# Kernel optimization log

Hardware: AMD Instinct MI355X
Metric: run time of the kernel (lower is better)

Reference implementation:

```python
import jax, jax.numpy as jnp
import numpy as np

HQ, HK, HD, DM = 16, 8, 128, 2048
GQA = HQ // HK
SCALE = HD ** -0.5


def _rotate_half(x):
    half = x.shape[-1] // 2
    return jnp.concatenate([-x[..., half:], x[..., :half]], axis=-1)


def _rope_tables(T, d, base=10000.0):
    inv_freq = 1.0 / (base ** (np.arange(0, d // 2, dtype=np.float32) * 2.0 / d))
    ang = np.arange(T, dtype=np.float32)[:, None] * inv_freq[None, :]  # [T, d/2]
    ang = np.concatenate([ang, ang], axis=-1)                          # [T, d]
    cos = jnp.asarray(np.cos(ang))[None, None]                         # [1,1,T,d]
    sin = jnp.asarray(np.sin(ang))[None, None]
    return cos, sin


def setup_inputs() -> dict:
    key = jax.random.key(0)
    ks = jax.random.split(key, 8)
    B, T, L = 1, 2048, 4
    x = jax.random.normal(ks[0], (B, T, DM), dtype=jnp.float32)
    depth_k = jax.random.normal(ks[1], (L, B, HK, T, HD), dtype=jnp.float32)
    depth_v = jax.random.normal(ks[2], (L, B, HK, T, HD), dtype=jnp.float32)
    cos, sin = _rope_tables(T, HD)
    Wq = jax.random.normal(ks[3], (DM, HQ * HD), dtype=jnp.float32) * 0.02
    Wk = jax.random.normal(ks[4], (DM, HK * HD), dtype=jnp.float32) * 0.02
    Wv = jax.random.normal(ks[5], (DM, HK * HD), dtype=jnp.float32) * 0.02
    Wo = jax.random.normal(ks[6], (HQ * HD, DM), dtype=jnp.float32) * 0.02
    return {"x": x, "depth_k": depth_k, "depth_v": depth_v, "cos": cos, "sin": sin,
            "Wq": Wq, "Wk": Wk, "Wv": Wv, "Wo": Wo}


def reference(x, depth_k, depth_v, cos, sin, Wq, Wk, Wv, Wo):
    B, T, D = x.shape
    # Projections -> [B, H, T, d]
    Q = (x @ Wq).reshape(B, T, HQ, HD).transpose(0, 2, 1, 3)
    K = (x @ Wk).reshape(B, T, HK, HD).transpose(0, 2, 1, 3)
    V = (x @ Wv).reshape(B, T, HK, HD).transpose(0, 2, 1, 3)
    # RoPE
    Q = Q * cos + _rotate_half(Q) * sin
    K = K * cos + _rotate_half(K) * sin
    # GQA expand (repeat_interleave along head axis)
    K_e = jnp.repeat(K, GQA, axis=1)
    V_e = jnp.repeat(V, GQA, axis=1)
    # Sequence logits with causal mask: [B, Hq, T, T]
    seq_logits = jnp.einsum('bhid,bhjd->bhij', Q, K_e) * SCALE
    causal = jnp.triu(jnp.ones((T, T), dtype=bool), k=1)
    seq_logits = jnp.where(causal[None, None], -jnp.inf, seq_logits)
    # Depth KVs: [L,B,Hk,T,d] -> [B,Hk,T,L,d] -> expand heads
    Kd = jnp.repeat(jnp.transpose(depth_k, (1, 2, 3, 0, 4)), GQA, axis=1)
    Vd = jnp.repeat(jnp.transpose(depth_v, (1, 2, 3, 0, 4)), GQA, axis=1)
    depth_logits = jnp.einsum('bhid,bhild->bhil', Q, Kd) * SCALE  # [B,Hq,T,L]
    # Joint softmax over sequence + depth positions
    combined = jnp.concatenate([seq_logits, depth_logits], axis=-1)
    weights = jax.nn.softmax(combined, axis=-1)
    seq_contrib = jnp.einsum('bhij,bhjd->bhid', weights[..., :T], V_e)
    depth_contrib = jnp.einsum('bhil,bhild->bhid', weights[..., T:], Vd)
    out = (seq_contrib + depth_contrib).transpose(0, 2, 1, 3).reshape(B, T, HQ * HD)
    return out @ Wo
```

## Files before the change

### kernel.cpp

```cpp
#include <hip/hip_runtime.h>
#include <hip/hip_bf16.h>
#include <math.h>

#define T_SEQ 2048
#define DMODEL 2048
#define NHQ 16
#define NHK 8
#define HDIM 128
#define NL 4
#define ATT_SCALE 0.08838834764831845f

typedef __attribute__((ext_vector_type(8))) short bf16x8;
typedef __attribute__((ext_vector_type(4))) float f32x4;

__device__ __forceinline__ float bf2f(short u) {
    union { float f; unsigned int i; } x;
    x.i = ((unsigned int)(unsigned short)u) << 16;
    return x.f;
}
__device__ __forceinline__ unsigned short f2bf(float f) {
    __hip_bfloat16 h = __float2bfloat16(f);
    return *reinterpret_cast<unsigned short*>(&h);
}
__device__ __forceinline__ void gload16(const void* g, void* l) {
    __builtin_amdgcn_global_load_lds(
        (const __attribute__((address_space(1))) void*)g,
        (__attribute__((address_space(3))) void*)l, 16, 0, 0);
}

__global__ __launch_bounds__(256) void cast_f32_bf16(
    const float* __restrict__ s, unsigned short* __restrict__ d)
{
    int i = blockIdx.x * 256 + threadIdx.x;
    float4 a = ((const float4*)s)[2 * i];
    float4 b = ((const float4*)s)[2 * i + 1];
    bf16x8 v;
    v[0] = (short)f2bf(a.x); v[1] = (short)f2bf(a.y);
    v[2] = (short)f2bf(a.z); v[3] = (short)f2bf(a.w);
    v[4] = (short)f2bf(b.x); v[5] = (short)f2bf(b.y);
    v[6] = (short)f2bf(b.z); v[7] = (short)f2bf(b.w);
    ((bf16x8*)d)[i] = v;
}

__global__ __launch_bounds__(256) void tcast(
    const float* __restrict__ src, unsigned short* __restrict__ dst,
    int Nsrc, int Ksrc, int dstOff)
{
    __shared__ float ls[64][65];
    const int k0 = blockIdx.x * 64, n0 = blockIdx.y * 64;
    const int tid = threadIdx.x;
    #pragma unroll
    for (int it = 0; it < 4; ++it) {
        int fi = tid + it * 256;
        int r = fi >> 4;
        int c = (fi & 15) * 4;
        float4 v = *(const float4*)&src[(size_t)(k0 + r) * Nsrc + n0 + c];
        ls[r][c] = v.x; ls[r][c + 1] = v.y; ls[r][c + 2] = v.z; ls[r][c + 3] = v.w;
    }
    __syncthreads();
    int n = tid & 63, kc = tid >> 6;
    bf16x8 v0, v1;
    #pragma unroll
    for (int j = 0; j < 8; ++j) v0[j] = (short)f2bf(ls[kc * 16 + j][n]);
    #pragma unroll
    for (int j = 0; j < 8; ++j) v1[j] = (short)f2bf(ls[kc * 16 + 8 + j][n]);
    size_t drow = (size_t)(dstOff + n0 + n) * Ksrc + k0 + kc * 16;
    *(bf16x8*)&dst[drow] = v0;
    *(bf16x8*)&dst[drow + 8] = v1;
}

__global__ __launch_bounds__(256, 4) void gemm_bt(
    const unsigned short* __restrict__ A, const unsigned short* __restrict__ Bt,
    float* __restrict__ Cf, unsigned short* __restrict__ Cq,
    unsigned short* __restrict__ Ck, unsigned short* __restrict__ Cv,
    int mode, int K)
{
    __shared__ char As[16384];
    __shared__ char Bs[8192];
    const int tid = threadIdx.x;
    const int wv = tid >> 6, lane = tid & 63;
    const int l15 = lane & 15, lg = lane >> 4;
    const int wm = wv >> 1, wn = wv & 1;
    const int bm = blockIdx.y * 128, bn = blockIdx.x * 64;

    f32x4 acc[4][2];
    #pragma unroll
    for (int i = 0; i < 4; ++i)
        #pragma unroll
        for (int j = 0; j < 2; ++j)
            acc[i][j] = (f32x4){0.f, 0.f, 0.f, 0.f};

    for (int k0 = 0; k0 < K; k0 += 64) {
        #pragma unroll
        for (int it = 0; it < 4; ++it) {
            int o = it * 4096 + tid * 16;
            int row = o >> 7;
            int sch = ((o >> 4) & 7) ^ (row & 7);
            gload16((const char*)A + ((((size_t)(bm + row) * K) + k0 + sch * 8) << 1),
                    As + it * 4096 + wv * 1024);
        }
        #pragma unroll
        for (int it = 0; it < 2; ++it) {
            int o = it * 4096 + tid * 16;
            int row = o >> 7;
            int sch = ((o >> 4) & 7) ^ (row & 7);
            gload16((const char*)Bt + ((((size_t)(bn + row) * K) + k0 + sch * 8) << 1),
                    Bs + it * 4096 + wv * 1024);
        }
        __syncthreads();
        #pragma unroll
        for (int kk = 0; kk < 2; ++kk) {
            bf16x8 av[4], bv[2];
            #pragma unroll
            for (int f = 0; f < 4; ++f) {
                int ra = wm * 64 + f * 16 + l15;
                av[f] = *(const bf16x8*)(As + ra * 128 + ((((kk << 2) | lg) ^ (ra & 7)) << 4));
            }
            #pragma unroll
            for (int f = 0; f < 2; ++f) {
                int rb = wn * 32 + f * 16 + l15;
                bv[f] = *(const bf16x8*)(Bs + rb * 128 + ((((kk << 2) | lg) ^ (rb & 7)) << 4));
            }
            #pragma unroll
            for (int mf = 0; mf < 4; ++mf)
                #pragma unroll
                for (int nf = 0; nf < 2; ++nf)
                    acc[mf][nf] = __builtin_amdgcn_mfma_f32_16x16x32_bf16(
                        av[mf], bv[nf], acc[mf][nf], 0, 0, 0);
        }
        __syncthreads();
    }

    #pragma unroll
    for (int mf = 0; mf < 4; ++mf) {
        int m0 = bm + wm * 64 + mf * 16 + lg * 4;
        #pragma unroll
        for (int nf = 0; nf < 2; ++nf) {
            int n0 = bn + wn * 32 + nf * 16 + l15;
            if (mode == 0) {
                #pragma unroll
                for (int r = 0; r < 4; ++r)
                    Cf[(size_t)(m0 + r) * 2048 + n0] = acc[mf][nf][r];
            } else if (n0 < 2048) {
                #pragma unroll
                for (int r = 0; r < 4; ++r)
                    Cq[(size_t)(m0 + r) * 2048 + n0] = f2bf(acc[mf][nf][r]);
            } else if (n0 < 3072) {
                #pragma unroll
                for (int r = 0; r < 4; ++r)
                    Ck[(size_t)(m0 + r) * 1024 + (n0 - 2048)] = f2bf(acc[mf][nf][r]);
            } else {
                ushort4 u;
                u.x = f2bf(acc[mf][nf][0]); u.y = f2bf(acc[mf][nf][1]);
                u.z = f2bf(acc[mf][nf][2]); u.w = f2bf(acc[mf][nf][3]);
                *(ushort4*)&Cv[(size_t)(n0 - 3072) * 2048 + m0] = u;
            }
        }
    }
}

__global__ __launch_bounds__(256) void rope_bf16(
    unsigned short* __restrict__ P, const float* __restrict__ cosT,
    const float* __restrict__ sinT, int H)
{
    int idx = blockIdx.x * 256 + threadIdx.x;
    int d = idx & 63;
    int h = (idx >> 6) % H;
    int t = idx / (64 * H);
    float c = cosT[t * HDIM + d];
    float s = sinT[t * HDIM + d];
    unsigned short* row = P + (size_t)t * (H * HDIM) + h * HDIM;
    float x0 = bf2f((short)row[d]), x1 = bf2f((short)row[d + 64]);
    row[d]      = f2bf(x0 * c - x1 * s);
    row[d + 64] = f2bf(x1 * c + x0 * s);
}

__global__ __launch_bounds__(256, 4) void attn_seg(
    const unsigned short* __restrict__ Qb, const unsigned short* __restrict__ Kb,
    const unsigned short* __restrict__ Vt,
    const float* __restrict__ Dk, const float* __restrict__ Dv,
    unsigned short* __restrict__ Opart, float2* __restrict__ mlpart)
{
    __shared__ char Ks[2][8192];
    __shared__ char Vs[2][8192];
    __shared__ char Ps[4096];

    const int bid = blockIdx.x;
    const int hk = bid & 7;
    const int idx = bid >> 3;
    const int hq = hk * 2 + (idx & 1);
    const int si = 79 - (idx >> 1);
    int qt, seg;
    if (si < 8)       { qt = si;            seg = 0; }
    else if (si < 24) { int v = si - 8;  qt = 8  + (v >> 1); seg = v & 1; }
    else if (si < 48) { int v = si - 24; int q3 = v / 3; qt = 16 + q3; seg = v - q3 * 3; }
    else              { int v = si - 48; qt = 24 + (v >> 2); seg = v & 3; }
    const int q0 = qt * 64;
    const int keys = q0 + 64;
    const int jbeg = seg * 512;
    const int jend = min(jbeg + 512, keys);

    const int tid = threadIdx.x;
    const int wv = tid >> 6, lane = tid & 63;
    const int l15 = lane & 15, lg = lane >> 4;
    const size_t DSTRIDE = (size_t)NHK * T_SEQ * HDIM;

    const int tq = q0 + wv * 16 + l15;
    const int qmax = q0 + wv * 16 + 15;

    bf16x8 qf[4];
    {
        const unsigned short* qrow = Qb + (size_t)tq * DMODEL + hq * HDIM;
        #pragma unroll
        for (int c = 0; c < 4; ++c)
            qf[c] = *(const bf16x8*)(qrow + c * 32 + lg * 8);
    }

    f32x4 oacc[8];
    #pragma unroll
    for (int dt = 0; dt < 8; ++dt) oacc[dt] = (f32x4){0.f, 0.f, 0.f, 0.f};
    float m = -1e30f, l = 0.f;

    #define STAGE(J0, BUF)                                                        \
        {                                                                         \
            _Pragma("unroll")                                                     \
            for (int it = 0; it < 2; ++it) {                                      \
                int o = it * 4096 + tid * 16;                                     \
                int rk = o >> 8, ck = (o >> 4) & 15;                              \
                gload16((const char*)Kb +                                         \
                        (((size_t)((J0) + rk) * 1024 + hk * 128 +                 \
                          ((ck ^ (rk & 7)) << 3)) << 1),                          \
                        Ks[BUF] + it * 4096 + wv * 1024);                         \
                int rv = o >> 6, cv = (o >> 4) & 3;                               \
                gload16((const char*)Vt +                                         \
                        (((size_t)(hk * 128 + rv) * 2048 + (J0) +                 \
                          ((cv ^ ((rv >> 1) & 3)) << 3)) << 1),                   \
                        Vs[BUF] + it * 4096 + wv * 1024);                         \
            }                                                                     \
        }

    STAGE(jbeg, 0);
    __syncthreads();
    int buf = 0;

    for (int j0 = jbeg; j0 < jend; j0 += 32) {
        if (j0 + 32 < jend) STAGE(j0 + 32, buf ^ 1);

        if (j0 <= qmax) {
            const char* ksb = Ks[buf];
            const char* vsb = Vs[buf];
            float p[2][4];
            #pragma unroll
            for (int s = 0; s < 2; ++s) {
                if (j0 + s * 16 <= qmax) {
                    f32x4 sa = (f32x4){0.f, 0.f, 0.f, 0.f};
                    int row = s * 16 + l15;
                    #pragma unroll
                    for (int c = 0; c < 4; ++c) {
                        int ch = (c * 4 + lg) ^ (row & 7);
                        bf16x8 kf = *(const bf16x8*)(ksb + row * 256 + ch * 16);
                        sa = __builtin_amdgcn_mfma_f32_16x16x32_bf16(kf, qf[c], sa, 0, 0, 0);
                    }
                    #pragma unroll
                    for (int r = 0; r < 4; ++r) {
                        int key = j0 + s * 16 + lg * 4 + r;
                        p[s][r] = (key <= tq) ? sa[r] * ATT_SCALE : -1e30f;
                    }
                } else {
                    #pragma unroll
                    for (int r = 0; r < 4; ++r) p[s][r] = -1e30f;
                }
            }
            float vmax = p[0][0];
            #pragma unroll
            for (int s = 0; s < 2; ++s)
                #pragma unroll
                for (int r = 0; r < 4; ++r) vmax = fmaxf(vmax, p[s][r]);
            vmax = fmaxf(vmax, __shfl_xor(vmax, 16));
            vmax = fmaxf(vmax, __shfl_xor(vmax, 32));
            if (!__all(vmax <= m + 8.0f)) {
                float mn = fmaxf(m, vmax);
                float rs = __expf(m - mn);
                m = mn;
                l *= rs;
                float rs_o[4];
                #pragma unroll
                for (int r = 0; r < 4; ++r) rs_o[r] = __shfl(rs, lg * 4 + r);
                #pragma unroll
                for (int dt = 0; dt < 8; ++dt)
                    #pragma unroll
                    for (int r = 0; r < 4; ++r) oacc[dt][r] *= rs_o[r];
            }
            float sum = 0.f;
            #pragma unroll
            for (int s = 0; s < 2; ++s)
                #pragma unroll
                for (int r = 0; r < 4; ++r) {
                    float pe = __expf(p[s][r] - m);
                    p[s][r] = pe;
                    sum += pe;
                }
            sum += __shfl_xor(sum, 16);
            sum += __shfl_xor(sum, 32);
            l += sum;

            char* pw = Ps + wv * 1024;
            #pragma unroll
            for (int s = 0; s < 2; ++s) {
                unsigned int lo = (unsigned int)f2bf(p[s][0]) |
                                  ((unsigned int)f2bf(p[s][1]) << 16);
                unsigned int hi = (unsigned int)f2bf(p[s][2]) |
                                  ((unsigned int)f2bf(p[s][3]) << 16);
                int kc = s * 2 + (lg >> 1);
                int ch = kc ^ ((l15 >> 1) & 3);
                uint2 u = make_uint2(lo, hi);
                *(uint2*)(pw + l15 * 64 + ch * 16 + (lg & 1) * 8) = u;
            }
            asm volatile("" ::: "memory");
            {
                bf16x8 pa = *(const bf16x8*)(pw + l15 * 64 + ((lg ^ ((l15 >> 1) & 3)) << 4));
                #pragma unroll
                for (int dt = 0; dt < 8; ++dt) {
                    int rv = dt * 16 + l15;
                    bf16x8 vf = *(const bf16x8*)(vsb + rv * 64 + ((lg ^ ((rv >> 1) & 3)) << 4));
                    oacc[dt] = __builtin_amdgcn_mfma_f32_16x16x32_bf16(pa, vf, oacc[dt], 0, 0, 0);
                }
            }
        }
        __syncthreads();
        buf ^= 1;
    }

    if (seg == (qt >> 3)) {
        float dl[NL];
        #pragma unroll
        for (int sl = 0; sl < NL; ++sl) {
            const float* kd = Dk + sl * DSTRIDE + ((size_t)hk * T_SEQ + tq) * HDIM;
            float a = 0.f;
            #pragma unroll
            for (int c = 0; c < 4; ++c) {
                const float* kc = kd + c * 32 + lg * 8;
                float4 v0 = *(const float4*)(kc);
                float4 v1 = *(const float4*)(kc + 4);
                a = fmaf(bf2f(qf[c][0]), v0.x, a);
                a = fmaf(bf2f(qf[c][1]), v0.y, a);
                a = fmaf(bf2f(qf[c][2]), v0.z, a);
                a = fmaf(bf2f(qf[c][3]), v0.w, a);
                a = fmaf(bf2f(qf[c][4]), v1.x, a);
                a = fmaf(bf2f(qf[c][5]), v1.y, a);
                a = fmaf(bf2f(qf[c][6]), v1.z, a);
                a = fmaf(bf2f(qf[c][7]), v1.w, a);
            }
            a += __shfl_xor(a, 16);
            a += __shfl_xor(a, 32);
            dl[sl] = a * ATT_SCALE;
        }
        float vm = fmaxf(fmaxf(dl[0], dl[1]), fmaxf(dl[2], dl[3]));
        float mn = fmaxf(m, vm);
        float rsd = __expf(m - mn);
        m = mn;
        float pd[NL];
        #pragma unroll
        for (int sl = 0; sl < NL; ++sl) pd[sl] = __expf(dl[sl] - mn);
        l = l * rsd + (pd[0] + pd[1] + pd[2] + pd[3]);
        float rs_o[4], pdo[NL][4];
        #pragma unroll
        for (int r = 0; r < 4; ++r) {
            rs_o[r] = __shfl(rsd, lg * 4 + r);
            #pragma unroll
            for (int sl = 0; sl < NL; ++sl) pdo[sl][r] = __shfl(pd[sl], lg * 4 + r);
        }
        #pragma unroll
        for (int r = 0; r < 4; ++r) {
            int t = q0 + wv * 16 + lg * 4 + r;
            #pragma unroll
            for (int dt = 0; dt < 8; ++dt) {
                const float* vb = Dv + ((size_t)hk * T_SEQ + t) * HDIM + dt * 16 + l15;
                float o = oacc[dt][r] * rs_o[r];
                o = fmaf(pdo[0][r], vb[0], o);
                o = fmaf(pdo[1][r], vb[DSTRIDE], o);
                o = fmaf(pdo[2][r], vb[2 * DSTRIDE], o);
                o = fmaf(pdo[3][r], vb[3 * DSTRIDE], o);
                oacc[dt][r] = o;
            }
        }
    }

    const int p = (hq * 32 + qt) * 4 + seg;
    unsigned short* op = Opart + (size_t)p * 8192;
    #pragma unroll
    for (int r = 0; r < 4; ++r) {
        unsigned short* orow = op + (wv * 16 + lg * 4 + r) * 128;
        #pragma unroll
        for (int dt = 0; dt < 8; ++dt)
            orow[dt * 16 + l15] = f2bf(oacc[dt][r]);
    }
    if (lg == 0) mlpart[p * 64 + wv * 16 + l15] = make_float2(m, l);
    #undef STAGE
}

__global__ __launch_bounds__(256) void attn_combine(
    const unsigned short* __restrict__ Opart, const float2* __restrict__ mlpart,
    unsigned short* __restrict__ AO)
{
    const int bid = blockIdx.x;
    const int hq = bid & 15;
    const int qt = bid >> 4;
    const int nseg = (qt >> 3) + 1;
    const int pbase = (hq * 32 + qt) * 4;
    const int tid = threadIdx.x;
    const int row = tid >> 2;
    const int dp = tid & 3;
    const int t = qt * 64 + row;

    float mi[4], li[4];
    float M = -1e30f;
    for (int i = 0; i < nseg; ++i) {
        float2 v = mlpart[(pbase + i) * 64 + row];
        mi[i] = v.x; li[i] = v.y;
        M = fmaxf(M, v.x);
    }
    float L = 0.f, w[4];
    for (int i = 0; i < nseg; ++i) {
        w[i] = __expf(mi[i] - M);
        L += w[i] * li[i];
    }
    float linv = 1.f / L;

    float o[32];
    #pragma unroll
    for (int j = 0; j < 32; ++j) o[j] = 0.f;
    for (int i = 0; i < nseg; ++i) {
        const unsigned short* opr = Opart + (size_t)(pbase + i) * 8192 + row * 128 + dp * 32;
        #pragma unroll
        for (int c = 0; c < 4; ++c) {
            bf16x8 v = *(const bf16x8*)(opr + c * 8);
            #pragma unroll
            for (int j = 0; j < 8; ++j)
                o[c * 8 + j] = fmaf(w[i], bf2f(v[j]), o[c * 8 + j]);
        }
    }
    unsigned short* orow = AO + (size_t)t * DMODEL + hq * HDIM + dp * 32;
    #pragma unroll
    for (int c = 0; c < 4; ++c) {
        bf16x8 v;
        #pragma unroll
        for (int j = 0; j < 8; ++j) v[j] = (short)f2bf(o[c * 8 + j] * linv);
        *(bf16x8*)(orow + c * 8) = v;
    }
}

extern "C" void kernel_launch(void* const* d_in, const int* in_sizes, int n_in,
                              void* d_out, int out_size, void* d_ws, size_t ws_size,
                              hipStream_t stream) {
    const float* x    = (const float*)d_in[0];
    const float* dk   = (const float*)d_in[1];
    const float* dv   = (const float*)d_in[2];
    const float* cosT = (const float*)d_in[3];
    const float* sinT = (const float*)d_in[4];
    const float* Wq   = (const float*)d_in[5];
    const float* Wk   = (const float*)d_in[6];
    const float* Wv   = (const float*)d_in[7];
    const float* Wo   = (const float*)d_in[8];
    float* out = (float*)d_out;

    unsigned short* xb    = (unsigned short*)d_ws;
    unsigned short* Qb    = xb + (size_t)4 * 1024 * 1024;
    unsigned short* Kb    = Qb + (size_t)4 * 1024 * 1024;
    unsigned short* Vt    = Kb + (size_t)2 * 1024 * 1024;
    unsigned short* WTp   = Vt + (size_t)2 * 1024 * 1024;
    unsigned short* WoT   = WTp + (size_t)8 * 1024 * 1024;
    unsigned short* Opart = WoT + (size_t)4 * 1024 * 1024;
    float2* mlpart = (float2*)(Opart + (size_t)2048 * 8192);
    unsigned short* AOb = xb;

    cast_f32_bf16<<<dim3(2048), 256, 0, stream>>>(x, xb);
    tcast<<<dim3(32, 32), 256, 0, stream>>>(Wq, WTp, 2048, 2048, 0);
    tcast<<<dim3(32, 16), 256, 0, stream>>>(Wk, WTp, 1024, 2048, 2048);
    tcast<<<dim3(32, 16), 256, 0, stream>>>(Wv, WTp, 1024, 2048, 3072);
    tcast<<<dim3(32, 32), 256, 0, stream>>>(Wo, WoT, 2048, 2048, 0);
    gemm_bt<<<dim3(64, 16), 256, 0, stream>>>(xb, WTp, nullptr, Qb, Kb, Vt, 1, DMODEL);
    rope_bf16<<<dim3(T_SEQ * NHQ * 64 / 256), 256, 0, stream>>>(Qb, cosT, sinT, NHQ);
    rope_bf16<<<dim3(T_SEQ * NHK * 64 / 256), 256, 0, stream>>>(Kb, cosT, sinT, NHK);
    attn_seg<<<dim3(1280), 256, 0, stream>>>(Qb, Kb, Vt, dk, dv, Opart, mlpart);
    attn_combine<<<dim3(512), 256, 0, stream>>>(Opart, mlpart, AOb);
    gemm_bt<<<dim3(32, 16), 256, 0, stream>>>(AOb, WoT, out, nullptr, nullptr, nullptr, 0, DMODEL);
}
```

Before: 177.2 us.

## Fuse prep kernels, split depth attention into own kernel, shuffle P instead of LDS

Merges the cast and four transpose-cast launches into one prep kernel, and the two RoPE launches into one. Depth-KV attention moves out of the tail of attn_seg into a separate depth_part kernel that writes a fifth partial slot, which the combine kernel merges. attn_seg now builds the P operand with cross-lane shuffles rather than an LDS round trip. It also skips the causal mask on fully visible tiles and raises occupancy to 5 blocks. In exchange there is an extra kernel launch, more partial-buffer traffic, and Opart now reuses the WTp workspace.

New measurement: 179.5 us. About the same (+1.3%).

```diff
diff --git a/kernel.cpp b/kernel.cpp
--- a/kernel.cpp
+++ b/kernel.cpp
@@ -28,34 +28,41 @@
         (__attribute__((address_space(3))) void*)l, 16, 0, 0);
 }
 
-__global__ __launch_bounds__(256) void cast_f32_bf16(
-    const float* __restrict__ s, unsigned short* __restrict__ d)
-{
-    int i = blockIdx.x * 256 + threadIdx.x;
-    float4 a = ((const float4*)s)[2 * i];
-    float4 b = ((const float4*)s)[2 * i + 1];
-    bf16x8 v;
-    v[0] = (short)f2bf(a.x); v[1] = (short)f2bf(a.y);
-    v[2] = (short)f2bf(a.z); v[3] = (short)f2bf(a.w);
-    v[4] = (short)f2bf(b.x); v[5] = (short)f2bf(b.y);
-    v[6] = (short)f2bf(b.z); v[7] = (short)f2bf(b.w);
-    ((bf16x8*)d)[i] = v;
-}
-
-__global__ __launch_bounds__(256) void tcast(
-    const float* __restrict__ src, unsigned short* __restrict__ dst,
-    int Nsrc, int Ksrc, int dstOff)
+__global__ __launch_bounds__(256) void prep(
+    const float* __restrict__ x, const float* __restrict__ Wq,
+    const float* __restrict__ Wk, const float* __restrict__ Wv,
+    const float* __restrict__ Wo,
+    unsigned short* __restrict__ xb, unsigned short* __restrict__ WTp,
+    unsigned short* __restrict__ WoT)
 {
     __shared__ float ls[64][65];
-    const int k0 = blockIdx.x * 64, n0 = blockIdx.y * 64;
-    const int tid = threadIdx.x;
+    const int bid = blockIdx.x, tid = threadIdx.x;
+    if (bid < 2048) {
+        int i = bid * 256 + tid;
+        float4 a = ((const float4*)x)[2 * i];
+        float4 b = ((const float4*)x)[2 * i + 1];
+        bf16x8 v;
+        v[0] = (short)f2bf(a.x); v[1] = (short)f2bf(a.y);
+        v[2] = (short)f2bf(a.z); v[3] = (short)f2bf(a.w);
+        v[4] = (short)f2bf(b.x); v[5] = (short)f2bf(b.y);
+        v[6] = (short)f2bf(b.z); v[7] = (short)f2bf(b.w);
+        ((bf16x8*)xb)[i] = v;
+        return;
+    }
+    int v = bid - 2048;
+    const float* src; unsigned short* dst; int Nsrc, dstOff, id;
+    if (v < 1024)      { src = Wq; dst = WTp; Nsrc = 2048; dstOff = 0;    id = v; }
+    else if (v < 1536) { src = Wk; dst = WTp; Nsrc = 1024; dstOff = 2048; id = v - 1024; }
+    else if (v < 2048) { src = Wv; dst = WTp; Nsrc = 1024; dstOff = 3072; id = v - 1536; }
+    else               { src = Wo; dst = WoT; Nsrc = 2048; dstOff = 0;    id = v - 2048; }
+    const int k0 = (id & 31) * 64, n0 = (id >> 5) * 64;
     #pragma unroll
     for (int it = 0; it < 4; ++it) {
         int fi = tid + it * 256;
         int r = fi >> 4;
         int c = (fi & 15) * 4;
-        float4 v = *(const float4*)&src[(size_t)(k0 + r) * Nsrc + n0 + c];
-        ls[r][c] = v.x; ls[r][c + 1] = v.y; ls[r][c + 2] = v.z; ls[r][c + 3] = v.w;
+        float4 w = *(const float4*)&src[(size_t)(k0 + r) * Nsrc + n0 + c];
+        ls[r][c] = w.x; ls[r][c + 1] = w.y; ls[r][c + 2] = w.z; ls[r][c + 3] = w.w;
     }
     __syncthreads();
     int n = tid & 63, kc = tid >> 6;
@@ -64,7 +71,7 @@
     for (int j = 0; j < 8; ++j) v0[j] = (short)f2bf(ls[kc * 16 + j][n]);
     #pragma unroll
     for (int j = 0; j < 8; ++j) v1[j] = (short)f2bf(ls[kc * 16 + 8 + j][n]);
-    size_t drow = (size_t)(dstOff + n0 + n) * Ksrc + k0 + kc * 16;
+    size_t drow = (size_t)(dstOff + n0 + n) * 2048 + k0 + kc * 16;
     *(bf16x8*)&dst[drow] = v0;
     *(bf16x8*)&dst[drow + 8] = v1;
 }
@@ -159,11 +166,14 @@
     }
 }
 
-__global__ __launch_bounds__(256) void rope_bf16(
-    unsigned short* __restrict__ P, const float* __restrict__ cosT,
-    const float* __restrict__ sinT, int H)
+__global__ __launch_bounds__(256) void rope2(
+    unsigned short* __restrict__ Qb, unsigned short* __restrict__ Kb,
+    const float* __restrict__ cosT, const float* __restrict__ sinT)
 {
     int idx = blockIdx.x * 256 + threadIdx.x;
+    unsigned short* P; int H;
+    if (idx < T_SEQ * NHQ * 64) { P = Qb; H = NHQ; }
+    else { idx -= T_SEQ * NHQ * 64; P = Kb; H = NHK; }
     int d = idx & 63;
     int h = (idx >> 6) % H;
     int t = idx / (64 * H);
@@ -175,15 +185,97 @@
     row[d + 64] = f2bf(x1 * c + x0 * s);
 }
 
-__global__ __launch_bounds__(256, 4) void attn_seg(
+__global__ __launch_bounds__(256) void depth_part(
+    const unsigned short* __restrict__ Qb,
+    const float* __restrict__ Dk, const float* __restrict__ Dv,
+    unsigned short* __restrict__ Opart, float2* __restrict__ mlpart)
+{
+    const int bid = blockIdx.x;
+    const int hk = bid & 7;
+    const int tc = bid >> 3;
+    const int tid = threadIdx.x;
+    const int row = tid >> 3;
+    const int dp = tid & 7;
+    const int t = tc * 32 + row;
+    const int qt = t >> 6, rowin = t & 63;
+    const size_t DSTRIDE = (size_t)NHK * T_SEQ * HDIM;
+    const size_t base = ((size_t)hk * T_SEQ + t) * HDIM + dp * 16;
+
+    float q[2][16];
+    #pragma unroll
+    for (int e = 0; e < 2; ++e) {
+        const unsigned short* qp = Qb + (size_t)t * DMODEL + (hk * 2 + e) * HDIM + dp * 16;
+        bf16x8 v0 = *(const bf16x8*)qp;
+        bf16x8 v1 = *(const bf16x8*)(qp + 8);
+        #pragma unroll
+        for (int j = 0; j < 8; ++j) { q[e][j] = bf2f(v0[j]); q[e][8 + j] = bf2f(v1[j]); }
+    }
+    float dl[2][NL];
+    #pragma unroll
+    for (int l = 0; l < NL; ++l) {
+        const float* kp = Dk + l * DSTRIDE + base;
+        float a0 = 0.f, a1 = 0.f;
+        #pragma unroll
+        for (int c = 0; c < 4; ++c) {
+            float4 k4 = *(const float4*)(kp + c * 4);
+            a0 = fmaf(q[0][c*4+0], k4.x, a0); a0 = fmaf(q[0][c*4+1], k4.y, a0);
+            a0 = fmaf(q[0][c*4+2], k4.z, a0); a0 = fmaf(q[0][c*4+3], k4.w, a0);
+            a1 = fmaf(q[1][c*4+0], k4.x, a1); a1 = fmaf(q[1][c*4+1], k4.y, a1);
+            a1 = fmaf(q[1][c*4+2], k4.z, a1); a1 = fmaf(q[1][c*4+3], k4.w, a1);
+        }
+        a0 += __shfl_xor(a0, 1); a0 += __shfl_xor(a0, 2); a0 += __shfl_xor(a0, 4);
+        a1 += __shfl_xor(a1, 1); a1 += __shfl_xor(a1, 2); a1 += __shfl_xor(a1, 4);
+        dl[0][l] = a0 * ATT_SCALE;
+        dl[1][l] = a1 * ATT_SCALE;
+    }
+    float m[2], ls[2], pd[2][NL];
+    #pragma unroll
+    for (int e = 0; e < 2; ++e) {
+        m[e] = fmaxf(fmaxf(dl[e][0], dl[e][1]), fmaxf(dl[e][2], dl[e][3]));
+        ls[e] = 0.f;
+        #pragma unroll
+        for (int l = 0; l < NL; ++l) { pd[e][l] = __expf(dl[e][l] - m[e]); ls[e] += pd[e][l]; }
+    }
+    float o[2][16];
+    #pragma unroll
+    for (int e = 0; e < 2; ++e)
+        #pragma unroll
+        for (int j = 0; j < 16; ++j) o[e][j] = 0.f;
+    #pragma unroll
+    for (int l = 0; l < NL; ++l) {
+        const float* vp = Dv + l * DSTRIDE + base;
+        #pragma unroll
+        for (int c = 0; c < 4; ++c) {
+            float4 v4 = *(const float4*)(vp + c * 4);
+            #pragma unroll
+            for (int e = 0; e < 2; ++e) {
+                o[e][c*4+0] = fmaf(pd[e][l], v4.x, o[e][c*4+0]);
+                o[e][c*4+1] = fmaf(pd[e][l], v4.y, o[e][c*4+1]);
+                o[e][c*4+2] = fmaf(pd[e][l], v4.z, o[e][c*4+2]);
+                o[e][c*4+3] = fmaf(pd[e][l], v4.w, o[e][c*4+3]);
+            }
+        }
+    }
+    #pragma unroll
+    for (int e = 0; e < 2; ++e) {
+        int pidx = ((hk * 2 + e) * 32 + qt) * 5 + 4;
+        unsigned short* dst = Opart + (size_t)pidx * 8192 + rowin * 128 + dp * 16;
+        bf16x8 w0, w1;
+        #pragma unroll
+        for (int j = 0; j < 8; ++j) { w0[j] = (short)f2bf(o[e][j]); w1[j] = (short)f2bf(o[e][8 + j]); }
+        *(bf16x8*)dst = w0;
+        *(bf16x8*)(dst + 8) = w1;
+        if (dp == 0) mlpart[pidx * 64 + rowin] = make_float2(m[e], ls[e]);
+    }
+}
+
+__global__ __launch_bounds__(256, 5) void attn_seg(
     const unsigned short* __restrict__ Qb, const unsigned short* __restrict__ Kb,
     const unsigned short* __restrict__ Vt,
-    const float* __restrict__ Dk, const float* __restrict__ Dv,
     unsigned short* __restrict__ Opart, float2* __restrict__ mlpart)
 {
     __shared__ char Ks[2][8192];
     __shared__ char Vs[2][8192];
-    __shared__ char Ps[4096];
 
     const int bid = blockIdx.x;
     const int hk = bid & 7;
@@ -203,10 +295,10 @@
     const int tid = threadIdx.x;
     const int wv = tid >> 6, lane = tid & 63;
     const int l15 = lane & 15, lg = lane >> 4;
-    const size_t DSTRIDE = (size_t)NHK * T_SEQ * HDIM;
 
     const int tq = q0 + wv * 16 + l15;
     const int qmax = q0 + wv * 16 + 15;
+    const int qmin = q0 + wv * 16;
 
     bf16x8 qf[4];
     {
@@ -249,6 +341,7 @@
         if (j0 <= qmax) {
             const char* ksb = Ks[buf];
             const char* vsb = Vs[buf];
+            const bool fullt = (j0 + 31 <= qmin);
             float p[2][4];
             #pragma unroll
             for (int s = 0; s < 2; ++s) {
@@ -264,7 +357,7 @@
                     #pragma unroll
                     for (int r = 0; r < 4; ++r) {
                         int key = j0 + s * 16 + lg * 4 + r;
-                        p[s][r] = (key <= tq) ? sa[r] * ATT_SCALE : -1e30f;
+                        p[s][r] = (fullt || key <= tq) ? sa[r] * ATT_SCALE : -1e30f;
                     }
                 } else {
                     #pragma unroll
@@ -304,89 +397,31 @@
             sum += __shfl_xor(sum, 32);
             l += sum;
 
-            char* pw = Ps + wv * 1024;
-            #pragma unroll
-            for (int s = 0; s < 2; ++s) {
-                unsigned int lo = (unsigned int)f2bf(p[s][0]) |
-                                  ((unsigned int)f2bf(p[s][1]) << 16);
-                unsigned int hi = (unsigned int)f2bf(p[s][2]) |
-                                  ((unsigned int)f2bf(p[s][3]) << 16);
-                int kc = s * 2 + (lg >> 1);
-                int ch = kc ^ ((l15 >> 1) & 3);
-                uint2 u = make_uint2(lo, hi);
-                *(uint2*)(pw + l15 * 64 + ch * 16 + (lg & 1) * 8) = u;
-            }
-            asm volatile("" ::: "memory");
-            {
-                bf16x8 pa = *(const bf16x8*)(pw + l15 * 64 + ((lg ^ ((l15 >> 1) & 3)) << 4));
-                #pragma unroll
-                for (int dt = 0; dt < 8; ++dt) {
-                    int rv = dt * 16 + l15;
-                    bf16x8 vf = *(const bf16x8*)(vsb + rv * 64 + ((lg ^ ((rv >> 1) & 3)) << 4));
-                    oacc[dt] = __builtin_amdgcn_mfma_f32_16x16x32_bf16(pa, vf, oacc[dt], 0, 0, 0);
-                }
+            unsigned int D00 = (unsigned int)f2bf(p[0][0]) | ((unsigned int)f2bf(p[0][1]) << 16);
+            unsigned int D01 = (unsigned int)f2bf(p[0][2]) | ((unsigned int)f2bf(p[0][3]) << 16);
+            unsigned int D10 = (unsigned int)f2bf(p[1][0]) | ((unsigned int)f2bf(p[1][1]) << 16);
+            unsigned int D11 = (unsigned int)f2bf(p[1][2]) | ((unsigned int)f2bf(p[1][3]) << 16);
+            int src0 = ((lg & 1) << 5) + l15;
+            int src1 = src0 + 16;
+            unsigned int a0 = __shfl(D00, src0), a1 = __shfl(D01, src0);
+            unsigned int a2 = __shfl(D00, src1), a3 = __shfl(D01, src1);
+            unsigned int b0 = __shfl(D10, src0), b1 = __shfl(D11, src0);
+            unsigned int b2 = __shfl(D10, src1), b3 = __shfl(D11, src1);
+            union { uint4 u; bf16x8 v; } pk;
+            pk.u = (lg & 2) ? make_uint4(b0, b1, b2, b3) : make_uint4(a0, a1, a2, a3);
+            bf16x8 pa = pk.v;
+            #pragma unroll
+            for (int dt = 0; dt < 8; ++dt) {
+                int rv = dt * 16 + l15;
+                bf16x8 vf = *(const bf16x8*)(vsb + rv * 64 + ((lg ^ ((rv >> 1) & 3)) << 4));
+                oacc[dt] = __builtin_amdgcn_mfma_f32_16x16x32_bf16(pa, vf, oacc[dt], 0, 0, 0);
             }
         }
         __syncthreads();
         buf ^= 1;
     }
 
-    if (seg == (qt >> 3)) {
-        float dl[NL];
-        #pragma unroll
-        for (int sl = 0; sl < NL; ++sl) {
-            const float* kd = Dk + sl * DSTRIDE + ((size_t)hk * T_SEQ + tq) * HDIM;
-            float a = 0.f;
-            #pragma unroll
-            for (int c = 0; c < 4; ++c) {
-                const float* kc = kd + c * 32 + lg * 8;
-                float4 v0 = *(const float4*)(kc);
-                float4 v1 = *(const float4*)(kc + 4);
-                a = fmaf(bf2f(qf[c][0]), v0.x, a);
-                a = fmaf(bf2f(qf[c][1]), v0.y, a);
-                a = fmaf(bf2f(qf[c][2]), v0.z, a);
-                a = fmaf(bf2f(qf[c][3]), v0.w, a);
-                a = fmaf(bf2f(qf[c][4]), v1.x, a);
-                a = fmaf(bf2f(qf[c][5]), v1.y, a);
-                a = fmaf(bf2f(qf[c][6]), v1.z, a);
-                a = fmaf(bf2f(qf[c][7]), v1.w, a);
-            }
-            a += __shfl_xor(a, 16);
-            a += __shfl_xor(a, 32);
-            dl[sl] = a * ATT_SCALE;
-        }
-        float vm = fmaxf(fmaxf(dl[0], dl[1]), fmaxf(dl[2], dl[3]));
-        float mn = fmaxf(m, vm);
-        float rsd = __expf(m - mn);
-        m = mn;
-        float pd[NL];
-        #pragma unroll
-        for (int sl = 0; sl < NL; ++sl) pd[sl] = __expf(dl[sl] - mn);
-        l = l * rsd + (pd[0] + pd[1] + pd[2] + pd[3]);
-        float rs_o[4], pdo[NL][4];
-        #pragma unroll
-        for (int r = 0; r < 4; ++r) {
-            rs_o[r] = __shfl(rsd, lg * 4 + r);
-            #pragma unroll
-            for (int sl = 0; sl < NL; ++sl) pdo[sl][r] = __shfl(pd[sl], lg * 4 + r);
-        }
-        #pragma unroll
-        for (int r = 0; r < 4; ++r) {
-            int t = q0 + wv * 16 + lg * 4 + r;
-            #pragma unroll
-            for (int dt = 0; dt < 8; ++dt) {
-                const float* vb = Dv + ((size_t)hk * T_SEQ + t) * HDIM + dt * 16 + l15;
-                float o = oacc[dt][r] * rs_o[r];
-                o = fmaf(pdo[0][r], vb[0], o);
-                o = fmaf(pdo[1][r], vb[DSTRIDE], o);
-                o = fmaf(pdo[2][r], vb[2 * DSTRIDE], o);
-                o = fmaf(pdo[3][r], vb[3 * DSTRIDE], o);
-                oacc[dt][r] = o;
-            }
-        }
-    }
-
-    const int p = (hq * 32 + qt) * 4 + seg;
+    const int p = (hq * 32 + qt) * 5 + seg;
     unsigned short* op = Opart + (size_t)p * 8192;
     #pragma unroll
     for (int r = 0; r < 4; ++r) {
@@ -407,21 +442,26 @@
     const int hq = bid & 15;
     const int qt = bid >> 4;
     const int nseg = (qt >> 3) + 1;
-    const int pbase = (hq * 32 + qt) * 4;
+    const int pbase = (hq * 32 + qt) * 5;
     const int tid = threadIdx.x;
     const int row = tid >> 2;
     const int dp = tid & 3;
     const int t = qt * 64 + row;
 
-    float mi[4], li[4];
+    int slots[5];
+    for (int i = 0; i < nseg; ++i) slots[i] = i;
+    slots[nseg] = 4;
+    const int cnt = nseg + 1;
+
+    float mi[5], li[5];
     float M = -1e30f;
-    for (int i = 0; i < nseg; ++i) {
-        float2 v = mlpart[(pbase + i) * 64 + row];
+    for (int i = 0; i < cnt; ++i) {
+        float2 v = mlpart[(pbase + slots[i]) * 64 + row];
         mi[i] = v.x; li[i] = v.y;
         M = fmaxf(M, v.x);
     }
-    float L = 0.f, w[4];
-    for (int i = 0; i < nseg; ++i) {
+    float L = 0.f, w[5];
+    for (int i = 0; i < cnt; ++i) {
         w[i] = __expf(mi[i] - M);
         L += w[i] * li[i];
     }
@@ -430,8 +470,9 @@
     float o[32];
     #pragma unroll
     for (int j = 0; j < 32; ++j) o[j] = 0.f;
-    for (int i = 0; i < nseg; ++i) {
-        const unsigned short* opr = Opart + (size_t)(pbase + i) * 8192 + row * 128 + dp * 32;
+    for (int i = 0; i < cnt; ++i) {
+        const unsigned short* opr =
+            Opart + (size_t)(pbase + slots[i]) * 8192 + row * 128 + dp * 32;
         #pragma unroll
         for (int c = 0; c < 4; ++c) {
             bf16x8 v = *(const bf16x8*)(opr + c * 8);
@@ -464,25 +505,21 @@
     const float* Wo   = (const float*)d_in[8];
     float* out = (float*)d_out;
 
-    unsigned short* xb    = (unsigned short*)d_ws;
-    unsigned short* Qb    = xb + (size_t)4 * 1024 * 1024;
-    unsigned short* Kb    = Qb + (size_t)4 * 1024 * 1024;
-    unsigned short* Vt    = Kb + (size_t)2 * 1024 * 1024;
-    unsigned short* WTp   = Vt + (size_t)2 * 1024 * 1024;
-    unsigned short* WoT   = WTp + (size_t)8 * 1024 * 1024;
-    unsigned short* Opart = WoT + (size_t)4 * 1024 * 1024;
-    float2* mlpart = (float2*)(Opart + (size_t)2048 * 8192);
+    unsigned short* xb  = (unsigned short*)d_ws;
+    unsigned short* Qb  = xb + (size_t)4 * 1024 * 1024;
+    unsigned short* Kb  = Qb + (size_t)4 * 1024 * 1024;
+    unsigned short* Vt  = Kb + (size_t)2 * 1024 * 1024;
+    unsigned short* WoT = Vt + (size_t)2 * 1024 * 1024;
+    unsigned short* WTp = WoT + (size_t)4 * 1024 * 1024;
+    unsigned short* Opart = WTp;
+    float2* mlpart = (float2*)(Opart + (size_t)2560 * 8192);
     unsigned short* AOb = xb;
 
-    cast_f32_bf16<<<dim3(2048), 256, 0, stream>>>(x, xb);
-    tcast<<<dim3(32, 32), 256, 0, stream>>>(Wq, WTp, 2048, 2048, 0);
-    tcast<<<dim3(32, 16), 256, 0, stream>>>(Wk, WTp, 1024, 2048, 2048);
-    tcast<<<dim3(32, 16), 256, 0, stream>>>(Wv, WTp, 1024, 2048, 3072);
-    tcast<<<dim3(32, 32), 256, 0, stream>>>(Wo, WoT, 2048, 2048, 0);
+    prep<<<dim3(5120), 256, 0, stream>>>(x, Wq, Wk, Wv, Wo, xb, WTp, WoT);
     gemm_bt<<<dim3(64, 16), 256, 0, stream>>>(xb, WTp, nullptr, Qb, Kb, Vt, 1, DMODEL);
-    rope_bf16<<<dim3(T_SEQ * NHQ * 64 / 256), 256, 0, stream>>>(Qb, cosT, sinT, NHQ);
-    rope_bf16<<<dim3(T_SEQ * NHK * 64 / 256), 256, 0, stream>>>(Kb, cosT, sinT, NHK);
-    attn_seg<<<dim3(1280), 256, 0, stream>>>(Qb, Kb, Vt, dk, dv, Opart, mlpart);
+    rope2<<<dim3(12288), 256, 0, stream>>>(Qb, Kb, cosT, sinT);
+    depth_part<<<dim3(512), 256, 0, stream>>>(Qb, dk, dv, Opart, mlpart);
+    attn_seg<<<dim3(1280), 256, 0, stream>>>(Qb, Kb, Vt, Opart, mlpart);
     attn_combine<<<dim3(512), 256, 0, stream>>>(Opart, mlpart, AOb);
     gemm_bt<<<dim3(32, 16), 256, 0, stream>>>(AOb, WoT, out, nullptr, nullptr, nullptr, 0, DMODEL);
 }
```
